# Kernel tuning notes

Hardware: AMD Instinct MI355X
Metric: run time of the kernel (lower is better)

Reference implementation:

```python
import jax, jax.numpy as jnp
import numpy as np

B, S, H, DH = 2, 2048, 16, 64
D = H * DH


def setup_inputs() -> dict:
    key = jax.random.key(0)
    ks = jax.random.split(key, 10)
    std = 0.02
    return {
        "hidden_states": jax.random.normal(ks[0], (B, S, D), jnp.float32),
        "mask": jax.random.randint(ks[1], (B, S), 0, 2, jnp.int64 if jax.config.jax_enable_x64 else jnp.int32),
        "Wq": jax.random.normal(ks[2], (D, D), jnp.float32) * std,
        "bq": jnp.zeros((D,), jnp.float32),
        "Wk": jax.random.normal(ks[3], (D, D), jnp.float32) * std,
        "bk": jnp.zeros((D,), jnp.float32),
        "Wv": jax.random.normal(ks[4], (D, D), jnp.float32) * std,
        "bv": jnp.zeros((D,), jnp.float32),
        "Wo": jax.random.normal(ks[5], (D, D), jnp.float32) * std,
        "bo": jnp.zeros((D,), jnp.float32),
    }


def _split_heads(x):
    # (B, S, H*DH) -> (B, H, S, DH)
    b, s, _ = x.shape
    return x.reshape(b, s, H, DH).transpose(0, 2, 1, 3)


def reference(hidden_states, mask, Wq, bq, Wk, bk, Wv, bv, Wo, bo):
    # Linear projections (torch nn.Linear: x @ W.T + b)
    q = _split_heads(hidden_states @ Wq.T + bq)
    k = _split_heads(hidden_states @ Wk.T + bk)
    v = _split_heads(hidden_states @ Wv.T + bv)

    scale = 1.0 / np.sqrt(DH).astype(np.float32)
    scores = jnp.einsum("bhqd,bhkd->bhqk", q, k) * scale  # (B,H,S,S)
    # mask out padded key positions (mask==0 -> -inf), broadcast over heads/queries
    scores = jnp.where(mask[:, None, None, :] == 0, -jnp.inf, scores)
    weights = jax.nn.softmax(scores, axis=-1)

    attended = jnp.einsum("bhqk,bhkd->bhqd", weights, v)  # (B,H,S,DH)
    merged = attended.transpose(0, 2, 1, 3).reshape(hidden_states.shape)  # (B,S,D)
    return merged @ Wo.T + bo
```

## Files before the change

### kernel.cpp

```cpp
#include <hip/hip_runtime.h>
#include <hip/hip_bf16.h>

typedef __bf16 bf16;
typedef __bf16 bf16x4 __attribute__((ext_vector_type(4)));
typedef __bf16 bf16x8 __attribute__((ext_vector_type(8)));
typedef float f32x4 __attribute__((ext_vector_type(4)));
typedef unsigned short u16x4 __attribute__((ext_vector_type(4)));

#define B_ 2
#define S_ 2048
#define H_ 16
#define DH_ 64
#define D_ 1024

#define WAIT_VMCNT0() asm volatile("s_waitcnt vmcnt(0)" ::: "memory")
#define WAIT_LGKM0()  asm volatile("s_waitcnt lgkmcnt(0)" ::: "memory")

__device__ __forceinline__ void gld_lds16(const bf16* g, bf16* l) {
    __builtin_amdgcn_global_load_lds(
        (__attribute__((address_space(1))) void*)g,
        (__attribute__((address_space(3))) void*)l, 16, 0, 0);
}

__device__ __forceinline__ bf16 f2bf(float x) {
    union { float f; unsigned u; } v; v.f = x;
    unsigned short h = (unsigned short)((v.u + 0x7FFF + ((v.u >> 16) & 1)) >> 16);
    return __builtin_bit_cast(bf16, h);
}

__device__ __forceinline__ unsigned cvtpk(float lo, float hi) {
    unsigned r;
    asm("v_cvt_pk_bf16_f32 %0, %1, %2" : "=v"(r) : "v"(lo), "v"(hi));
    return r;
}

__device__ __forceinline__ void pl32swap(unsigned &a, unsigned &b) {
    asm("v_permlane32_swap_b32 %0, %1" : "+v"(a), "+v"(b));
}
__device__ __forceinline__ void pl16swap(unsigned &a, unsigned &b) {
    asm("v_permlane16_swap_b32 %0, %1" : "+v"(a), "+v"(b));
}

__global__ __launch_bounds__(256) void cvt_kernel(
    const float* __restrict__ hs,
    const float* __restrict__ Wq, const float* __restrict__ Wk,
    const float* __restrict__ Wv, const float* __restrict__ Wo,
    bf16* __restrict__ hsb, bf16* __restrict__ wqkv, bf16* __restrict__ wob)
{
    int i = (blockIdx.x * 256 + threadIdx.x) * 4;
    const float* src;
    bf16* dst;
    if (i < 4194304) {
        src = hs + i; dst = hsb + i;
    } else if (i < 7340032) {
        int off = i - 4194304;
        int which = off >> 20;
        int within = off & 1048575;
        src = (which == 0 ? Wq : which == 1 ? Wk : Wv) + within;
        dst = wqkv + off;
    } else {
        int off = i - 7340032;
        src = Wo + off; dst = wob + off;
    }
    float4 v = *(const float4*)src;
    bf16x4 o = { (bf16)v.x, (bf16)v.y, (bf16)v.z, (bf16)v.w };
    *(bf16x4*)dst = o;
}

__global__ __launch_bounds__(256, 3) void gemm_bt(
    const bf16* __restrict__ A, const bf16* __restrict__ Bm,
    const float* __restrict__ b0, const float* __restrict__ b1,
    const float* __restrict__ b2,
    bf16* __restrict__ Qo, bf16* __restrict__ Ko, bf16* __restrict__ Vt)
{
    const int K = 1024;
    __shared__ __attribute__((aligned(16))) bf16 sA[128 * 64];
    __shared__ __attribute__((aligned(16))) bf16 sB[128 * 64];

    int tid = threadIdx.x;
    int wave = tid >> 6, lane = tid & 63;
    int quad = lane >> 4, l16 = lane & 15;
    int m0 = blockIdx.x * 128;
    int n0 = blockIdx.y * 128;
    int wm = (wave & 1) * 64, wn = (wave >> 1) * 64;
    int fs = l16 & 7;

    f32x4 acc[4][4];
#pragma unroll
    for (int i = 0; i < 4; i++)
#pragma unroll
        for (int j = 0; j < 4; j++) acc[i][j] = (f32x4){0.f, 0.f, 0.f, 0.f};

    for (int k0 = 0; k0 < K; k0 += 64) {
#pragma unroll
        for (int i = 0; i < 4; i++) {
            int c = tid + i * 256;
            int row = c >> 3;
            int kc = ((c & 7) ^ (row & 7)) * 8;
            gld_lds16(A + (size_t)(m0 + row) * K + k0 + kc, &sA[c * 8]);
            gld_lds16(Bm + (size_t)(n0 + row) * K + k0 + kc, &sB[c * 8]);
        }
        WAIT_VMCNT0();
        __syncthreads();

#pragma unroll
        for (int kp = 0; kp < 2; kp++) {
            bf16x8 af[4], bfr[4];
#pragma unroll
            for (int i = 0; i < 4; i++)
                af[i] = *(const bf16x8*)&sA[(wm + i * 16 + l16) * 64 + (((kp * 4 + quad) ^ fs) * 8)];
#pragma unroll
            for (int j = 0; j < 4; j++)
                bfr[j] = *(const bf16x8*)&sB[(wn + j * 16 + l16) * 64 + (((kp * 4 + quad) ^ fs) * 8)];
#pragma unroll
            for (int i = 0; i < 4; i++)
#pragma unroll
                for (int j = 0; j < 4; j++)
                    acc[i][j] = __builtin_amdgcn_mfma_f32_16x16x32_bf16(
                        af[i], bfr[j], acc[i][j], 0, 0, 0);
        }
        __syncthreads();
    }

    const float QSCALE = 0.125f * 1.44269504088896340736f;
#pragma unroll
    for (int j = 0; j < 4; j++) {
        int n = n0 + wn + j * 16 + l16;
        int region = n >> 10;
        int nn = n & 1023;
        int h = nn >> 6, d = nn & 63;
        float bias = (region == 0 ? b0 : region == 1 ? b1 : b2)[nn];
#pragma unroll
        for (int i = 0; i < 4; i++) {
            int mb = m0 + wm + i * 16 + quad * 4;
            int b = mb >> 11, s = mb & 2047;
            int bh = b * H_ + h;
            if (region == 2) {
                bf16x4 pk = { f2bf(acc[i][j][0] + bias), f2bf(acc[i][j][1] + bias),
                              f2bf(acc[i][j][2] + bias), f2bf(acc[i][j][3] + bias) };
                *(bf16x4*)&Vt[((size_t)bh * DH_ + d) * S_ + s] = pk;
            } else {
#pragma unroll
                for (int r = 0; r < 4; r++) {
                    float v = acc[i][j][r] + bias;
                    if (region == 0)
                        Qo[((size_t)bh * S_ + s + r) * DH_ + d] = f2bf(v * QSCALE);
                    else
                        Ko[((size_t)bh * S_ + s + r) * DH_ + d] = f2bf(v);
                }
            }
        }
    }
}

__global__ __launch_bounds__(256, 2) void gemm_out(
    const bf16* __restrict__ A, const bf16* __restrict__ Bm,
    const float* __restrict__ bias0, float* __restrict__ Co)
{
    const int K = 1024;
    __shared__ __attribute__((aligned(16))) bf16 sA[128 * 64];
    __shared__ __attribute__((aligned(16))) bf16 sB[64 * 64];

    int tid = threadIdx.x;
    int wave = tid >> 6, lane = tid & 63;
    int quad = lane >> 4, l16 = lane & 15;
    int m0 = blockIdx.x * 128;
    int n0 = blockIdx.y * 64;
    int wm = (wave & 1) * 64, wn = (wave >> 1) * 32;
    int fs = l16 & 7;

    f32x4 acc[4][2];
#pragma unroll
    for (int i = 0; i < 4; i++)
#pragma unroll
        for (int j = 0; j < 2; j++) acc[i][j] = (f32x4){0.f, 0.f, 0.f, 0.f};

    for (int k0 = 0; k0 < K; k0 += 64) {
#pragma unroll
        for (int i = 0; i < 4; i++) {
            int c = tid + i * 256;
            int row = c >> 3;
            int kc = ((c & 7) ^ (row & 7)) * 8;
            gld_lds16(A + (size_t)(m0 + row) * K + k0 + kc, &sA[c * 8]);
        }
#pragma unroll
        for (int i = 0; i < 2; i++) {
            int c = tid + i * 256;
            int row = c >> 3;
            int kc = ((c & 7) ^ (row & 7)) * 8;
            gld_lds16(Bm + (size_t)(n0 + row) * K + k0 + kc, &sB[c * 8]);
        }
        WAIT_VMCNT0();
        __syncthreads();

#pragma unroll
        for (int kp = 0; kp < 2; kp++) {
            bf16x8 af[4], bfr[2];
#pragma unroll
            for (int i = 0; i < 4; i++)
                af[i] = *(const bf16x8*)&sA[(wm + i * 16 + l16) * 64 + (((kp * 4 + quad) ^ fs) * 8)];
#pragma unroll
            for (int j = 0; j < 2; j++)
                bfr[j] = *(const bf16x8*)&sB[(wn + j * 16 + l16) * 64 + (((kp * 4 + quad) ^ fs) * 8)];
#pragma unroll
            for (int i = 0; i < 4; i++)
#pragma unroll
                for (int j = 0; j < 2; j++)
                    acc[i][j] = __builtin_amdgcn_mfma_f32_16x16x32_bf16(
                        af[i], bfr[j], acc[i][j], 0, 0, 0);
        }
        __syncthreads();
    }

#pragma unroll
    for (int j = 0; j < 2; j++) {
        int n = n0 + wn + j * 16 + l16;
        float bias = bias0[n];
#pragma unroll
        for (int i = 0; i < 4; i++)
#pragma unroll
            for (int r = 0; r < 4; r++) {
                int m = m0 + wm + i * 16 + quad * 4 + r;
                Co[(size_t)m * D_ + n] = acc[i][j][r] + bias;
            }
    }
}

__global__ __launch_bounds__(256, 4) void attn_kernel(
    const bf16* __restrict__ Q, const bf16* __restrict__ Kg,
    const bf16* __restrict__ Vt, const int* __restrict__ mask,
    bf16* __restrict__ Og)
{
    __shared__ __attribute__((aligned(16))) bf16 sK[128 * 64];
    __shared__ __attribute__((aligned(16))) bf16 sV[64 * 128];
    __shared__ __attribute__((aligned(16))) unsigned short sMadd[S_];
    __shared__ float sPsumR[64];
    __shared__ float sPsumF[64];

    int tid = threadIdx.x;
    int wave = tid >> 6, lane = tid & 63;
    int quad = lane >> 4, l16 = lane & 15;
    int bh = blockIdx.y;
    int b = bh >> 4;
    int q0 = blockIdx.x * 64;
    int f8 = l16 & 7;
    int qh = wave & 1;
    int kh = wave >> 1;

    const bf16* Qb = Q + (size_t)bh * S_ * DH_;
    const bf16* Kb = Kg + (size_t)bh * S_ * DH_;
    const bf16* Vb = Vt + (size_t)bh * DH_ * S_;

    {
        int base = b * S_ + tid * 8;
        int4 m0 = *(const int4*)&mask[base];
        int4 m1 = *(const int4*)&mask[base + 4];
        u16x4 e0 = { (unsigned short)(m0.x ? 0 : 0xF149),
                     (unsigned short)(m0.y ? 0 : 0xF149),
                     (unsigned short)(m0.z ? 0 : 0xF149),
                     (unsigned short)(m0.w ? 0 : 0xF149) };
        u16x4 e1 = { (unsigned short)(m1.x ? 0 : 0xF149),
                     (unsigned short)(m1.y ? 0 : 0xF149),
                     (unsigned short)(m1.z ? 0 : 0xF149),
                     (unsigned short)(m1.w ? 0 : 0xF149) };
        *(u16x4*)&sMadd[tid * 8] = e0;
        *(u16x4*)&sMadd[tid * 8 + 4] = e1;
    }

    bf16x8 aq[2][2];
#pragma unroll
    for (int qt = 0; qt < 2; qt++) {
        int qrow = q0 + qh * 32 + qt * 16 + l16;
        aq[qt][0] = *(const bf16x8*)&Qb[(size_t)qrow * DH_ + quad * 8];
        aq[qt][1] = *(const bf16x8*)&Qb[(size_t)qrow * DH_ + 32 + quad * 8];
    }

    f32x4 o[2][4];
#pragma unroll
    for (int i = 0; i < 2; i++)
#pragma unroll
        for (int j = 0; j < 4; j++) o[i][j] = (f32x4){0.f, 0.f, 0.f, 0.f};
    float psum[2] = {0.f, 0.f};

    for (int kt = 0; kt < S_; kt += 128) {
#pragma unroll
        for (int i = 0; i < 8; i++) {
            int c = tid + i * 256;
            if (c < 1024) {
                int row = c >> 3;
                int g = (c & 7) ^ (row & 7);
                gld_lds16(&Kb[(size_t)(kt + row) * DH_ + g * 8], &sK[c * 8]);
            } else {
                int cv = c - 1024;
                int row = cv >> 4;
                int g = (cv & 15) ^ (row & 15);
                gld_lds16(&Vb[(size_t)row * S_ + kt + g * 8], &sV[cv * 8]);
            }
        }
        WAIT_VMCNT0();
        __syncthreads();

#pragma unroll
        for (int pass = 0; pass < 2; pass++) {
            unsigned w01[2][2], w23[2][2];
#pragma unroll
            for (int mtl = 0; mtl < 2; mtl++) {
                int keyrow = kh * 64 + pass * 32 + mtl * 16;
                bf16x8 ak0 = *(const bf16x8*)&sK[(keyrow + l16) * 64 + ((quad ^ f8) * 8)];
                bf16x8 ak1 = *(const bf16x8*)&sK[(keyrow + l16) * 64 + (((quad + 4) ^ f8) * 8)];
                u16x4 mm = *(const u16x4*)&sMadd[kt + keyrow + quad * 4];
                float ma0 = __builtin_bit_cast(float, (unsigned)mm.x << 16);
                float ma1 = __builtin_bit_cast(float, (unsigned)mm.y << 16);
                float ma2 = __builtin_bit_cast(float, (unsigned)mm.z << 16);
                float ma3 = __builtin_bit_cast(float, (unsigned)mm.w << 16);
#pragma unroll
                for (int qt = 0; qt < 2; qt++) {
                    f32x4 c = (f32x4){0.f, 0.f, 0.f, 0.f};
                    c = __builtin_amdgcn_mfma_f32_16x16x32_bf16(ak0, aq[qt][0], c, 0, 0, 0);
                    c = __builtin_amdgcn_mfma_f32_16x16x32_bf16(ak1, aq[qt][1], c, 0, 0, 0);
                    float p0 = __builtin_amdgcn_exp2f(c[0] + ma0);
                    float p1 = __builtin_amdgcn_exp2f(c[1] + ma1);
                    float p2 = __builtin_amdgcn_exp2f(c[2] + ma2);
                    float p3 = __builtin_amdgcn_exp2f(c[3] + ma3);
                    psum[qt] += (p0 + p1) + (p2 + p3);
                    w01[qt][mtl] = cvtpk(p0, p1);
                    w23[qt][mtl] = cvtpk(p2, p3);
                }
            }

            bf16x8 ap[2];
#pragma unroll
            for (int qt = 0; qt < 2; qt++) {
                unsigned r0 = w01[qt][0], r2 = w01[qt][1];
                pl32swap(r0, r2); pl16swap(r0, r2);
                unsigned r1 = w23[qt][0], r3 = w23[qt][1];
                pl32swap(r1, r3); pl16swap(r1, r3);
                union { unsigned u[4]; bf16x8 v; } U;
                U.u[0] = r0; U.u[1] = r1; U.u[2] = r2; U.u[3] = r3;
                ap[qt] = U.v;
            }

#pragma unroll
            for (int dt = 0; dt < 4; dt++) {
                int g = (kh * 8 + pass * 4 + quad) ^ l16;
                bf16x8 bv = *(const bf16x8*)&sV[(dt * 16 + l16) * 128 + g * 8];
#pragma unroll
                for (int qt = 0; qt < 2; qt++)
                    o[qt][dt] = __builtin_amdgcn_mfma_f32_16x16x32_bf16(ap[qt], bv, o[qt][dt], 0, 0, 0);
            }
        }
        __syncthreads();
    }

#pragma unroll
    for (int qt = 0; qt < 2; qt++) {
        float v = psum[qt];
        v += __shfl_xor(v, 16);
        v += __shfl_xor(v, 32);
        psum[qt] = v;
    }

    __syncthreads();
    float* sRed = (wave == 2) ? (float*)sK : (float*)sV;
    if (wave >= 2) {
#pragma unroll
        for (int qt = 0; qt < 2; qt++)
#pragma unroll
            for (int dt = 0; dt < 4; dt++)
                *(f32x4*)&sRed[((qt * 4 + dt) * 64 + lane) * 4] = o[qt][dt];
#pragma unroll
        for (int qt = 0; qt < 2; qt++)
            sPsumR[(wave - 2) * 32 + qt * 16 + l16] = psum[qt];
    }
    __syncthreads();
    if (wave < 2) {
        float* src = (wave == 0) ? (float*)sK : (float*)sV;
#pragma unroll
        for (int qt = 0; qt < 2; qt++)
#pragma unroll
            for (int dt = 0; dt < 4; dt++)
                o[qt][dt] += *(const f32x4*)&src[((qt * 4 + dt) * 64 + lane) * 4];
#pragma unroll
        for (int qt = 0; qt < 2; qt++)
            sPsumF[wave * 32 + qt * 16 + l16] = psum[qt] + sPsumR[wave * 32 + qt * 16 + l16];
        WAIT_LGKM0();
        int h = bh & 15;
#pragma unroll
        for (int qt = 0; qt < 2; qt++) {
            float4 ps = *(const float4*)&sPsumF[wave * 32 + qt * 16 + quad * 4];
            float rcp[4] = { 1.f / ps.x, 1.f / ps.y, 1.f / ps.z, 1.f / ps.w };
#pragma unroll
            for (int r = 0; r < 4; r++) {
                int s = q0 + wave * 32 + qt * 16 + quad * 4 + r;
#pragma unroll
                for (int dt = 0; dt < 4; dt++) {
                    int d = dt * 16 + l16;
                    Og[((size_t)(b * S_ + s)) * D_ + h * 64 + d] = f2bf(o[qt][dt][r] * rcp[r]);
                }
            }
        }
    }
}

extern "C" void kernel_launch(void* const* d_in, const int* in_sizes, int n_in,
                              void* d_out, int out_size, void* d_ws, size_t ws_size,
                              hipStream_t stream) {
    const float* hs = (const float*)d_in[0];
    const int* mask = (const int*)d_in[1];
    const float* Wq = (const float*)d_in[2];
    const float* bq = (const float*)d_in[3];
    const float* Wk = (const float*)d_in[4];
    const float* bk = (const float*)d_in[5];
    const float* Wv = (const float*)d_in[6];
    const float* bv = (const float*)d_in[7];
    const float* Wo = (const float*)d_in[8];
    const float* bo = (const float*)d_in[9];
    float* out = (float*)d_out;

    char* ws = (char*)d_ws;
    bf16* hsb  = (bf16*)(ws);
    bf16* wqkv = (bf16*)(ws + ((size_t)8 << 20));
    bf16* wob  = (bf16*)(ws + ((size_t)14 << 20));
    bf16* Qw   = (bf16*)(ws + ((size_t)16 << 20));
    bf16* Kw   = (bf16*)(ws + ((size_t)24 << 20));
    bf16* Vtw  = (bf16*)(ws + ((size_t)32 << 20));
    bf16* attn = (bf16*)(ws + ((size_t)40 << 20));

    cvt_kernel<<<8192, 256, 0, stream>>>(hs, Wq, Wk, Wv, Wo, hsb, wqkv, wob);
    gemm_bt<<<dim3(32, 24), 256, 0, stream>>>(hsb, wqkv, bq, bk, bv,
                                              Qw, Kw, Vtw);
    attn_kernel<<<dim3(32, 32), 256, 0, stream>>>(Qw, Kw, Vtw, mask, attn);
    gemm_out<<<dim3(32, 16), 256, 0, stream>>>(attn, wob, bo, out);
}
```

Measured before the change: 189.2 us.

## Double-buffer K/V tiles and widen attention blocks to 128 queries with 8 waves

```diff
diff --git a/kernel.cpp b/kernel.cpp
--- a/kernel.cpp
+++ b/kernel.cpp
@@ -226,178 +226,153 @@
     }
 }
 
-__global__ __launch_bounds__(256, 4) void attn_kernel(
+__global__ __launch_bounds__(512, 4) void attn_kernel(
     const bf16* __restrict__ Q, const bf16* __restrict__ Kg,
     const bf16* __restrict__ Vt, const int* __restrict__ mask,
     bf16* __restrict__ Og)
 {
-    __shared__ __attribute__((aligned(16))) bf16 sK[128 * 64];
-    __shared__ __attribute__((aligned(16))) bf16 sV[64 * 128];
+    __shared__ __attribute__((aligned(16))) bf16 sK[2][128 * 64];
+    __shared__ __attribute__((aligned(16))) bf16 sV[2][64 * 128];
     __shared__ __attribute__((aligned(16))) unsigned short sMadd[S_];
-    __shared__ float sPsumR[64];
-    __shared__ float sPsumF[64];
+    __shared__ float sPsumW[128];
 
     int tid = threadIdx.x;
     int wave = tid >> 6, lane = tid & 63;
     int quad = lane >> 4, l16 = lane & 15;
     int bh = blockIdx.y;
     int b = bh >> 4;
-    int q0 = blockIdx.x * 64;
+    int q0 = blockIdx.x * 128;
     int f8 = l16 & 7;
-    int qh = wave & 1;
-    int kh = wave >> 1;
 
     const bf16* Qb = Q + (size_t)bh * S_ * DH_;
     const bf16* Kb = Kg + (size_t)bh * S_ * DH_;
     const bf16* Vb = Vt + (size_t)bh * DH_ * S_;
 
     {
-        int base = b * S_ + tid * 8;
-        int4 m0 = *(const int4*)&mask[base];
-        int4 m1 = *(const int4*)&mask[base + 4];
+        int4 m0 = *(const int4*)&mask[b * S_ + tid * 4];
         u16x4 e0 = { (unsigned short)(m0.x ? 0 : 0xF149),
                      (unsigned short)(m0.y ? 0 : 0xF149),
                      (unsigned short)(m0.z ? 0 : 0xF149),
                      (unsigned short)(m0.w ? 0 : 0xF149) };
-        u16x4 e1 = { (unsigned short)(m1.x ? 0 : 0xF149),
-                     (unsigned short)(m1.y ? 0 : 0xF149),
-                     (unsigned short)(m1.z ? 0 : 0xF149),
-                     (unsigned short)(m1.w ? 0 : 0xF149) };
-        *(u16x4*)&sMadd[tid * 8] = e0;
-        *(u16x4*)&sMadd[tid * 8 + 4] = e1;
-    }
-
-    bf16x8 aq[2][2];
-#pragma unroll
-    for (int qt = 0; qt < 2; qt++) {
-        int qrow = q0 + qh * 32 + qt * 16 + l16;
-        aq[qt][0] = *(const bf16x8*)&Qb[(size_t)qrow * DH_ + quad * 8];
-        aq[qt][1] = *(const bf16x8*)&Qb[(size_t)qrow * DH_ + 32 + quad * 8];
-    }
-
-    f32x4 o[2][4];
-#pragma unroll
-    for (int i = 0; i < 2; i++)
-#pragma unroll
-        for (int j = 0; j < 4; j++) o[i][j] = (f32x4){0.f, 0.f, 0.f, 0.f};
-    float psum[2] = {0.f, 0.f};
-
-    for (int kt = 0; kt < S_; kt += 128) {
-#pragma unroll
-        for (int i = 0; i < 8; i++) {
-            int c = tid + i * 256;
-            if (c < 1024) {
+        *(u16x4*)&sMadd[tid * 4] = e0;
+    }
+
+    bf16x8 aq[2];
+    {
+        int qrow = q0 + wave * 16 + l16;
+        aq[0] = *(const bf16x8*)&Qb[(size_t)qrow * DH_ + quad * 8];
+        aq[1] = *(const bf16x8*)&Qb[(size_t)qrow * DH_ + 32 + quad * 8];
+    }
+
+    f32x4 o[4];
+#pragma unroll
+    for (int j = 0; j < 4; j++) o[j] = (f32x4){0.f, 0.f, 0.f, 0.f};
+    float psum = 0.f;
+
+#pragma unroll
+    for (int i = 0; i < 2; i++) {
+        int c = tid + i * 512;
+        int row = c >> 3;
+        int g = (c & 7) ^ (row & 7);
+        gld_lds16(&Kb[(size_t)row * DH_ + g * 8], &sK[0][c * 8]);
+    }
+#pragma unroll
+    for (int i = 0; i < 2; i++) {
+        int cv = tid + i * 512;
+        int row = cv >> 4;
+        int g = (cv & 15) ^ (row & 15);
+        gld_lds16(&Vb[(size_t)row * S_ + g * 8], &sV[0][cv * 8]);
+    }
+    WAIT_VMCNT0();
+    __syncthreads();
+
+    for (int kti = 0; kti < 16; kti++) {
+        int kt = kti * 128;
+        int cur = kti & 1;
+
+        if (kti < 15) {
+            int ktn = kt + 128;
+#pragma unroll
+            for (int i = 0; i < 2; i++) {
+                int c = tid + i * 512;
                 int row = c >> 3;
                 int g = (c & 7) ^ (row & 7);
-                gld_lds16(&Kb[(size_t)(kt + row) * DH_ + g * 8], &sK[c * 8]);
-            } else {
-                int cv = c - 1024;
+                gld_lds16(&Kb[(size_t)(ktn + row) * DH_ + g * 8], &sK[cur ^ 1][c * 8]);
+            }
+#pragma unroll
+            for (int i = 0; i < 2; i++) {
+                int cv = tid + i * 512;
                 int row = cv >> 4;
                 int g = (cv & 15) ^ (row & 15);
-                gld_lds16(&Vb[(size_t)row * S_ + kt + g * 8], &sV[cv * 8]);
-            }
-        }
-        WAIT_VMCNT0();
-        __syncthreads();
-
-#pragma unroll
-        for (int pass = 0; pass < 2; pass++) {
-            unsigned w01[2][2], w23[2][2];
-#pragma unroll
-            for (int mtl = 0; mtl < 2; mtl++) {
-                int keyrow = kh * 64 + pass * 32 + mtl * 16;
-                bf16x8 ak0 = *(const bf16x8*)&sK[(keyrow + l16) * 64 + ((quad ^ f8) * 8)];
-                bf16x8 ak1 = *(const bf16x8*)&sK[(keyrow + l16) * 64 + (((quad + 4) ^ f8) * 8)];
+                gld_lds16(&Vb[(size_t)row * S_ + ktn + g * 8], &sV[cur ^ 1][cv * 8]);
+            }
+        }
+
+        const bf16* sKc = sK[cur];
+        const bf16* sVc = sV[cur];
+
+#pragma unroll
+        for (int ks = 0; ks < 4; ks++) {
+            unsigned w01[2], w23[2];
+#pragma unroll
+            for (int m = 0; m < 2; m++) {
+                int keyrow = ks * 32 + m * 16;
+                bf16x8 ak0 = *(const bf16x8*)&sKc[(keyrow + l16) * 64 + ((quad ^ f8) * 8)];
+                bf16x8 ak1 = *(const bf16x8*)&sKc[(keyrow + l16) * 64 + (((quad + 4) ^ f8) * 8)];
                 u16x4 mm = *(const u16x4*)&sMadd[kt + keyrow + quad * 4];
-                float ma0 = __builtin_bit_cast(float, (unsigned)mm.x << 16);
-                float ma1 = __builtin_bit_cast(float, (unsigned)mm.y << 16);
-                float ma2 = __builtin_bit_cast(float, (unsigned)mm.z << 16);
-                float ma3 = __builtin_bit_cast(float, (unsigned)mm.w << 16);
-#pragma unroll
-                for (int qt = 0; qt < 2; qt++) {
-                    f32x4 c = (f32x4){0.f, 0.f, 0.f, 0.f};
-                    c = __builtin_amdgcn_mfma_f32_16x16x32_bf16(ak0, aq[qt][0], c, 0, 0, 0);
-                    c = __builtin_amdgcn_mfma_f32_16x16x32_bf16(ak1, aq[qt][1], c, 0, 0, 0);
-                    float p0 = __builtin_amdgcn_exp2f(c[0] + ma0);
-                    float p1 = __builtin_amdgcn_exp2f(c[1] + ma1);
-                    float p2 = __builtin_amdgcn_exp2f(c[2] + ma2);
-                    float p3 = __builtin_amdgcn_exp2f(c[3] + ma3);
-                    psum[qt] += (p0 + p1) + (p2 + p3);
-                    w01[qt][mtl] = cvtpk(p0, p1);
-                    w23[qt][mtl] = cvtpk(p2, p3);
-                }
-            }
-
-            bf16x8 ap[2];
-#pragma unroll
-            for (int qt = 0; qt < 2; qt++) {
-                unsigned r0 = w01[qt][0], r2 = w01[qt][1];
-                pl32swap(r0, r2); pl16swap(r0, r2);
-                unsigned r1 = w23[qt][0], r3 = w23[qt][1];
-                pl32swap(r1, r3); pl16swap(r1, r3);
-                union { unsigned u[4]; bf16x8 v; } U;
-                U.u[0] = r0; U.u[1] = r1; U.u[2] = r2; U.u[3] = r3;
-                ap[qt] = U.v;
-            }
+                f32x4 c;
+                c[0] = __builtin_bit_cast(float, (unsigned)mm.x << 16);
+                c[1] = __builtin_bit_cast(float, (unsigned)mm.y << 16);
+                c[2] = __builtin_bit_cast(float, (unsigned)mm.z << 16);
+                c[3] = __builtin_bit_cast(float, (unsigned)mm.w << 16);
+                c = __builtin_amdgcn_mfma_f32_16x16x32_bf16(ak0, aq[0], c, 0, 0, 0);
+                c = __builtin_amdgcn_mfma_f32_16x16x32_bf16(ak1, aq[1], c, 0, 0, 0);
+                float p0 = __builtin_amdgcn_exp2f(c[0]);
+                float p1 = __builtin_amdgcn_exp2f(c[1]);
+                float p2 = __builtin_amdgcn_exp2f(c[2]);
+                float p3 = __builtin_amdgcn_exp2f(c[3]);
+                psum += (p0 + p1) + (p2 + p3);
+                w01[m] = cvtpk(p0, p1);
+                w23[m] = cvtpk(p2, p3);
+            }
+
+            unsigned r0 = w01[0], r2 = w01[1];
+            pl32swap(r0, r2); pl16swap(r0, r2);
+            unsigned r1 = w23[0], r3 = w23[1];
+            pl32swap(r1, r3); pl16swap(r1, r3);
+            union { unsigned u[4]; bf16x8 v; } U;
+            U.u[0] = r0; U.u[1] = r1; U.u[2] = r2; U.u[3] = r3;
+            bf16x8 ap = U.v;
 
 #pragma unroll
             for (int dt = 0; dt < 4; dt++) {
-                int g = (kh * 8 + pass * 4 + quad) ^ l16;
-                bf16x8 bv = *(const bf16x8*)&sV[(dt * 16 + l16) * 128 + g * 8];
-#pragma unroll
-                for (int qt = 0; qt < 2; qt++)
-                    o[qt][dt] = __builtin_amdgcn_mfma_f32_16x16x32_bf16(ap[qt], bv, o[qt][dt], 0, 0, 0);
-            }
-        }
-        __syncthreads();
-    }
-
-#pragma unroll
-    for (int qt = 0; qt < 2; qt++) {
-        float v = psum[qt];
-        v += __shfl_xor(v, 16);
-        v += __shfl_xor(v, 32);
-        psum[qt] = v;
-    }
-
-    __syncthreads();
-    float* sRed = (wave == 2) ? (float*)sK : (float*)sV;
-    if (wave >= 2) {
-#pragma unroll
-        for (int qt = 0; qt < 2; qt++)
-#pragma unroll
-            for (int dt = 0; dt < 4; dt++)
-                *(f32x4*)&sRed[((qt * 4 + dt) * 64 + lane) * 4] = o[qt][dt];
-#pragma unroll
-        for (int qt = 0; qt < 2; qt++)
-            sPsumR[(wave - 2) * 32 + qt * 16 + l16] = psum[qt];
-    }
-    __syncthreads();
-    if (wave < 2) {
-        float* src = (wave == 0) ? (float*)sK : (float*)sV;
-#pragma unroll
-        for (int qt = 0; qt < 2; qt++)
-#pragma unroll
-            for (int dt = 0; dt < 4; dt++)
-                o[qt][dt] += *(const f32x4*)&src[((qt * 4 + dt) * 64 + lane) * 4];
-#pragma unroll
-        for (int qt = 0; qt < 2; qt++)
-            sPsumF[wave * 32 + qt * 16 + l16] = psum[qt] + sPsumR[wave * 32 + qt * 16 + l16];
-        WAIT_LGKM0();
-        int h = bh & 15;
-#pragma unroll
-        for (int qt = 0; qt < 2; qt++) {
-            float4 ps = *(const float4*)&sPsumF[wave * 32 + qt * 16 + quad * 4];
-            float rcp[4] = { 1.f / ps.x, 1.f / ps.y, 1.f / ps.z, 1.f / ps.w };
-#pragma unroll
-            for (int r = 0; r < 4; r++) {
-                int s = q0 + wave * 32 + qt * 16 + quad * 4 + r;
-#pragma unroll
-                for (int dt = 0; dt < 4; dt++) {
-                    int d = dt * 16 + l16;
-                    Og[((size_t)(b * S_ + s)) * D_ + h * 64 + d] = f2bf(o[qt][dt][r] * rcp[r]);
-                }
-            }
+                bf16x8 bv = *(const bf16x8*)&sVc[(dt * 16 + l16) * 128 + (((ks * 4 + quad) ^ l16) * 8)];
+                o[dt] = __builtin_amdgcn_mfma_f32_16x16x32_bf16(ap, bv, o[dt], 0, 0, 0);
+            }
+        }
+
+        if (kti < 15) {
+            WAIT_VMCNT0();
+            __syncthreads();
+        }
+    }
+
+    psum += __shfl_xor(psum, 16);
+    psum += __shfl_xor(psum, 32);
+
+    sPsumW[wave * 16 + l16] = psum;
+    WAIT_LGKM0();
+    float4 ps = *(const float4*)&sPsumW[wave * 16 + quad * 4];
+    float rcp[4] = { 1.f / ps.x, 1.f / ps.y, 1.f / ps.z, 1.f / ps.w };
+
+    int h = bh & 15;
+#pragma unroll
+    for (int r = 0; r < 4; r++) {
+        int s = q0 + wave * 16 + quad * 4 + r;
+#pragma unroll
+        for (int dt = 0; dt < 4; dt++) {
+            int d = dt * 16 + l16;
+            Og[((size_t)(b * S_ + s)) * D_ + h * 64 + d] = f2bf(o[dt][r] * rcp[r]);
         }
     }
 }
@@ -429,6 +404,6 @@
     cvt_kernel<<<8192, 256, 0, stream>>>(hs, Wq, Wk, Wv, Wo, hsb, wqkv, wob);
     gemm_bt<<<dim3(32, 24), 256, 0, stream>>>(hsb, wqkv, bq, bk, bv,
                                               Qw, Kw, Vtw);
-    attn_kernel<<<dim3(32, 32), 256, 0, stream>>>(Qw, Kw, Vtw, mask, attn);
+    attn_kernel<<<dim3(16, 32), 512, 0, stream>>>(Qw, Kw, Vtw, mask, attn);
     gemm_out<<<dim3(32, 16), 256, 0, stream>>>(attn, wob, bo, out);
 }
```

After: 203.0 us. 1.07x slower.
